# Kernel tuning notes

Measured on AMD Instinct MI355X. Metric: run time of the kernel, lower is better.

Reference implementation:

```python
import jax, jax.numpy as jnp
import numpy as np

EPS = 1e-5

def rmsnorm(x, g):
    var = jnp.mean(jnp.square(x), axis=-1, keepdims=True)
    return x * jax.lax.rsqrt(var + EPS) * g

def setup_inputs() -> dict:
    key = jax.random.key(0)
    ks = jax.random.split(key, 8)
    B, S, T, D = 2, 2048, 2048, 1024
    H, HKV, HD = 16, 4, 64
    std = 0.02
    return {
        "x": jax.random.normal(ks[0], (B, S, D), jnp.float32),
        "kv": jax.random.normal(ks[1], (B, T, D), jnp.float32),
        "wq": jax.random.normal(ks[2], (H * HD, D), jnp.float32) * std,
        "wk": jax.random.normal(ks[3], (HKV * HD, D), jnp.float32) * std,
        "wv": jax.random.normal(ks[4], (HKV * HD, D), jnp.float32) * std,
        "wo": jax.random.normal(ks[5], (D, H * HD), jnp.float32) * std,
        "gq": jnp.ones((D,), jnp.float32),
        "gkv": jnp.ones((D,), jnp.float32),
    }

def reference(x, kv, wq, wk, wv, wo, gq, gkv):
    B, S, D = x.shape
    T = kv.shape[1]
    H, HKV, HD = 16, 4, 64
    R = H // HKV  # heads per kv group
    xn = rmsnorm(x, gq)
    kvn = rmsnorm(kv, gkv)
    # projections
    q = (xn @ wq.T).reshape(B, S, HKV, R, HD)   # grouped query heads
    k = (kvn @ wk.T).reshape(B, T, HKV, HD)
    v = (kvn @ wv.T).reshape(B, T, HKV, HD)
    scale = 1.0 / jnp.sqrt(jnp.float32(HD))
    # block-mask is None -> full dense cross attention; GQA via broadcast einsum
    scores = jnp.einsum('bsgrd,btgd->bgrst', q, k) * scale  # [B,HKV,R,S,T]
    probs = jax.nn.softmax(scores, axis=-1)
    out = jnp.einsum('bgrst,btgd->bsgrd', probs, v)  # [B,S,HKV,R,HD]
    out = out.reshape(B, S, H * HD) @ wo.T
    return x + out
```

## Files before the change

kernel.cpp:

```cpp
#include <hip/hip_runtime.h>

#define DEV __device__ __forceinline__

typedef __attribute__((ext_vector_type(8))) _Float16 h8;
typedef __attribute__((ext_vector_type(4))) float f32x4;

DEV unsigned short f2h(float f) {
  union { _Float16 h[2]; unsigned short u[2]; } v;
  v.h[0] = (_Float16)f;
  return v.u[0];
}

DEV float h2f(unsigned short u) {
  union { _Float16 h[2]; unsigned short u[2]; } v;
  v.u[0] = u;
  return (float)v.h[0];
}

DEV unsigned int pack2h(float a, float b) {
  union { __fp16 __attribute__((ext_vector_type(2))) p; unsigned int u; } v;
  v.p = __builtin_amdgcn_cvt_pkrtz(a, b);
  return v.u;
}

DEV void async_load16(const void* g, void* l) {
  __builtin_amdgcn_global_load_lds(
      (const __attribute__((address_space(1))) void*)g,
      (__attribute__((address_space(3))) void*)l,
      16, 0, 0);
}


__global__ __launch_bounds__(256) void prep(const float* __restrict__ x,
                                            const float* __restrict__ kv,
                                            const float* __restrict__ wq,
                                            const float* __restrict__ wk,
                                            const float* __restrict__ wv,
                                            const float* __restrict__ wo,
                                            const float* __restrict__ gq,
                                            const float* __restrict__ gkv,
                                            unsigned short* __restrict__ wqb,
                                            unsigned short* __restrict__ wkvb,
                                            unsigned short* __restrict__ wob,
                                            unsigned short* __restrict__ xn,
                                            unsigned short* __restrict__ kvn,
                                            float qscale) {
  const int b = blockIdx.x, tid = threadIdx.x;
  if (b < 2560) {
    const float* src;
    unsigned short* dst;
    float sc = 1.0f;
    int base;
    if (b < 1024) { src = wq; dst = wqb; sc = qscale; base = b; }
    else if (b < 1280) { src = wk; dst = wkvb; base = b - 1024; }
    else if (b < 1536) { src = wv; dst = wkvb + 262144; base = b - 1280; }
    else { src = wo; dst = wob; base = b - 1536; }
    const int i = (base * 256 + tid) * 4;
    float4 v = *(const float4*)&src[i];
    ushort4 o;
    o.x = f2h(v.x * sc); o.y = f2h(v.y * sc);
    o.z = f2h(v.z * sc); o.w = f2h(v.w * sc);
    *(ushort4*)&dst[i] = o;
    return;
  }
  int row = b - 2560;
  const float* src;
  const float* g;
  unsigned short* dst;
  if (row < 4096) { src = x; g = gq; dst = xn; }
  else { row -= 4096; src = kv; g = gkv; dst = kvn; }
  const float* xr = src + (size_t)row * 1024;
  float4 v = *(const float4*)&xr[tid * 4];
  float ss = v.x * v.x + v.y * v.y + v.z * v.z + v.w * v.w;
  ss += __shfl_xor(ss, 32); ss += __shfl_xor(ss, 16);
  ss += __shfl_xor(ss, 8);  ss += __shfl_xor(ss, 4);
  ss += __shfl_xor(ss, 2);  ss += __shfl_xor(ss, 1);
  __shared__ float red[4];
  if ((tid & 63) == 0) red[tid >> 6] = ss;
  __syncthreads();
  float tot = red[0] + red[1] + red[2] + red[3];
  float inv = rsqrtf(tot * (1.0f / 1024.0f) + 1e-5f);
  float4 gv = *(const float4*)&g[tid * 4];
  ushort4 o;
  o.x = f2h(v.x * inv * gv.x); o.y = f2h(v.y * inv * gv.y);
  o.z = f2h(v.z * inv * gv.z); o.w = f2h(v.w * inv * gv.w);
  *(ushort4*)&dst[(size_t)row * 1024 + tid * 4] = o;
}

#define GEMM_KLOOP(A_, W_, m0_, n0_, Al_, Bl_, acc_)                                   \
  for (int kk = 0; kk < 1024; kk += 64) {                                              \
    __syncthreads();                                                                   \
    _Pragma("unroll") for (int j = 0; j < 6; ++j) {                                    \
      const int idx = w * 6 + j;                                                       \
      if (idx < 16) {                                                                  \
        const int p = idx >> 3, rb = (idx & 7) * 16;                                   \
        async_load16(A_ + (size_t)(m0_ + rb + r4) * 1024 + kk + p * 32 + c4s,          \
                     &Al_[p][rb * 32]);                                                \
      } else {                                                                         \
        const int ib = idx - 16;                                                       \
        const int p = ib >> 2, rb = (ib & 3) * 16;                                     \
        async_load16(W_ + (size_t)(n0_ + rb + r4) * 1024 + kk + p * 32 + c4s,          \
                     &Bl_[p][rb * 32]);                                                \
      }                                                                                \
    }                                                                                  \
    __syncthreads();                                                                   \
    _Pragma("unroll") for (int kc = 0; kc < 2; ++kc) {                                 \
      h8 af[4], bf[2];                                                                 \
      _Pragma("unroll") for (int mi = 0; mi < 4; ++mi)                                 \
        af[mi] = *(const h8*)&Al_[kc][(wm0 + mi * 16 + ln) * 32 + qs8];                \
      _Pragma("unroll") for (int ni = 0; ni < 2; ++ni)                                 \
        bf[ni] = *(const h8*)&Bl_[kc][(wn0 + ni * 16 + ln) * 32 + qs8];                \
      _Pragma("unroll") for (int mi = 0; mi < 4; ++mi)                                 \
        _Pragma("unroll") for (int ni = 0; ni < 2; ++ni)                               \
          acc_[mi][ni] =                                                               \
              __builtin_amdgcn_mfma_f32_16x16x32_f16(af[mi], bf[ni], acc_[mi][ni],     \
                                                     0, 0, 0);                         \
    }                                                                                  \
  }

__global__ __launch_bounds__(256) void proj_gemm(const unsigned short* __restrict__ xn,
                                                 const unsigned short* __restrict__ kvn,
                                                 const unsigned short* __restrict__ wqb,
                                                 const unsigned short* __restrict__ wkvb,
                                                 unsigned short* __restrict__ qb,
                                                 unsigned short* __restrict__ kb,
                                                 unsigned short* __restrict__ vTb) {
  __shared__ unsigned short Al[2][128 * 32];
  __shared__ unsigned short Bl[2][64 * 32];
  const int tid = threadIdx.x;
  const int w = tid >> 6, l = tid & 63;
  const int quad = l >> 4, ln = l & 15;
  const int wm0 = (w >> 1) * 64, wn0 = (w & 1) * 32;
  const int r4 = l >> 2;
  const int c4s = (((l & 3) ^ ((l >> 3) & 3))) * 8;
  const int qs8 = (quad ^ ((l >> 1) & 3)) * 8;

  int z = blockIdx.x;
  const unsigned short *A, *W;
  int m0, n0, isq;
  if (z < 512) {
    A = xn; W = wqb; isq = 1;
    m0 = (((z >> 7) << 3) + (z & 7)) * 128;
    n0 = ((z >> 3) & 15) * 64;
  } else {
    z -= 512; A = kvn; W = wkvb; isq = 0;
    m0 = (((z >> 6) << 3) + (z & 7)) * 128;
    n0 = ((z >> 3) & 7) * 64;
  }

  f32x4 acc[4][2] = {};
  GEMM_KLOOP(A, W, m0, n0, Al, Bl, acc)

#pragma unroll
  for (int mi = 0; mi < 4; ++mi)
#pragma unroll
    for (int ni = 0; ni < 2; ++ni)
#pragma unroll
      for (int r = 0; r < 4; ++r) {
        const int row = m0 + wm0 + mi * 16 + quad * 4 + r;
        const int col = n0 + wn0 + ni * 16 + ln;
        const unsigned short v = f2h(acc[mi][ni][r]);
        if (isq) {
          qb[((size_t)row << 10) + col] = v;
        } else if (col < 256) {
          kb[(size_t)row * 256 + col] = v;
        } else {
          const int c2 = col - 256, gg = c2 >> 6, dd = c2 & 63;
          const int bb = row >> 11, t = row & 2047;
          vTb[((size_t)((bb * 4 + gg) * 64 + dd) << 11) + t] = v;
        }
      }
}

__global__ __launch_bounds__(256) void o_gemm(const unsigned short* __restrict__ attb,
                                              const unsigned short* __restrict__ wob,
                                              const float* __restrict__ x,
                                              float* __restrict__ out) {
  __shared__ unsigned short Al[2][128 * 32];
  __shared__ unsigned short Bl[2][64 * 32];
  const int tid = threadIdx.x;
  const int w = tid >> 6, l = tid & 63;
  const int quad = l >> 4, ln = l & 15;
  const int wm0 = (w >> 1) * 64, wn0 = (w & 1) * 32;
  const int r4 = l >> 2;
  const int c4s = (((l & 3) ^ ((l >> 3) & 3))) * 8;
  const int qs8 = (quad ^ ((l >> 1) & 3)) * 8;

  const int z = blockIdx.x;
  const int m0 = (((z >> 7) << 3) + (z & 7)) * 128;
  const int n0 = ((z >> 3) & 15) * 64;

  f32x4 acc[4][2] = {};
  GEMM_KLOOP(attb, wob, m0, n0, Al, Bl, acc)

#pragma unroll
  for (int mi = 0; mi < 4; ++mi)
#pragma unroll
    for (int ni = 0; ni < 2; ++ni)
#pragma unroll
      for (int r = 0; r < 4; ++r) {
        const int row = m0 + wm0 + mi * 16 + quad * 4 + r;
        const int col = n0 + wn0 + ni * 16 + ln;
        const size_t idx = ((size_t)row << 10) + col;
        out[idx] = x[idx] + acc[mi][ni][r];
      }
}

__global__ __launch_bounds__(256, 4) void flash_attn(const unsigned short* __restrict__ q,
                                                     const unsigned short* __restrict__ k,
                                                     const unsigned short* __restrict__ vT,
                                                     unsigned short* __restrict__ o0,
                                                     unsigned short* __restrict__ o1,
                                                     float* __restrict__ l0p,
                                                     float* __restrict__ l1p) {
  __shared__ unsigned short KV[4][64 * 32];
  __shared__ unsigned short P[4 * 32 * 72];

  const int tid = threadIdx.x;
  const int w = tid >> 6, l = tid & 63;
  const int quad = l >> 4, ln = l & 15;
  const int s0 = blockIdx.x * 128;
  const int h = blockIdx.y, g = h >> 2;
  const int b = blockIdx.z >> 1, ts = blockIdx.z & 1;
  const int tbase = ts << 10;

  unsigned short* Opart = ts ? o1 : o0;
  float* lpart = ts ? l1p : l0p;

  h8 qf[2][2];
#pragma unroll
  for (int nq = 0; nq < 2; ++nq)
#pragma unroll
    for (int c = 0; c < 2; ++c)
      qf[nq][c] = *(const h8*)&q[(((size_t)(b * 2048 + s0 + w * 32 + nq * 16 + ln)) << 10) +
                                 h * 64 + c * 32 + quad * 8];

  f32x4 oacc[2][4] = {};
  float lsum[2] = {0.0f, 0.0f};

  const unsigned short* kbase = k + ((size_t)(b * 2048)) * 256 + g * 64;
  const unsigned short* vbase = vT + (((size_t)(b * 4 + g) * 64) << 11);
  unsigned short* Pw = &P[w * 32 * 72];

  const int r4 = l >> 2;
  const int c4s = (((l & 3) ^ ((l >> 3) & 3))) * 8;
  const int qs8 = (quad ^ ((l >> 1) & 3)) * 8;

  for (int it = 0; it < 16; ++it) {
    const int t0 = tbase + it * 64;
    __syncthreads();
#pragma unroll
    for (int c = 0; c < 4; ++c) {
      const unsigned short* src;
      if (w < 2)
        src = kbase + (size_t)(t0 + c * 16 + r4) * 256 + w * 32 + c4s;
      else
        src = vbase + (((size_t)(c * 16 + r4)) << 11) + t0 + (w - 2) * 32 + c4s;
      async_load16(src, &KV[w][c * 512]);
    }
    __syncthreads();

    f32x4 st[2][4];
#pragma unroll
    for (int tb = 0; tb < 4; ++tb) {
      h8 ka = *(const h8*)&KV[0][tb * 512 + ln * 32 + qs8];
      h8 kb2 = *(const h8*)&KV[1][tb * 512 + ln * 32 + qs8];
#pragma unroll
      for (int nq = 0; nq < 2; ++nq) {
        f32x4 s = {};
        s = __builtin_amdgcn_mfma_f32_16x16x32_f16(ka, qf[nq][0], s, 0, 0, 0);
        s = __builtin_amdgcn_mfma_f32_16x16x32_f16(kb2, qf[nq][1], s, 0, 0, 0);
        st[nq][tb] = s;
      }
    }

#pragma unroll
    for (int nq = 0; nq < 2; ++nq) {
#pragma unroll
      for (int tb = 0; tb < 4; ++tb) {
        float p0 = __builtin_amdgcn_exp2f(fminf(st[nq][tb][0], 14.0f));
        float p1 = __builtin_amdgcn_exp2f(fminf(st[nq][tb][1], 14.0f));
        float p2 = __builtin_amdgcn_exp2f(fminf(st[nq][tb][2], 14.0f));
        float p3 = __builtin_amdgcn_exp2f(fminf(st[nq][tb][3], 14.0f));
        lsum[nq] += (p0 + p1) + (p2 + p3);
        uint2 pk; pk.x = pack2h(p0, p1); pk.y = pack2h(p2, p3);
        *(uint2*)&Pw[(nq * 16 + ln) * 72 + tb * 16 + quad * 4] = pk;
      }
    }

    asm volatile("s_waitcnt lgkmcnt(0)" ::: "memory");

#pragma unroll
    for (int c = 0; c < 2; ++c) {
      h8 pf0 = *(const h8*)&Pw[(0 * 16 + ln) * 72 + c * 32 + quad * 8];
      h8 pf1 = *(const h8*)&Pw[(1 * 16 + ln) * 72 + c * 32 + quad * 8];
#pragma unroll
      for (int cb = 0; cb < 4; ++cb) {
        h8 vb = *(const h8*)&KV[2 + c][cb * 512 + ln * 32 + qs8];
        oacc[0][cb] = __builtin_amdgcn_mfma_f32_16x16x32_f16(pf0, vb, oacc[0][cb], 0, 0, 0);
        oacc[1][cb] = __builtin_amdgcn_mfma_f32_16x16x32_f16(pf1, vb, oacc[1][cb], 0, 0, 0);
      }
    }
  }

#pragma unroll
  for (int nq = 0; nq < 2; ++nq) {
    lsum[nq] += __shfl_xor(lsum[nq], 16);
    lsum[nq] += __shfl_xor(lsum[nq], 32);
    if (l < 16)
      lpart[(size_t)(b * 2048 + s0 + w * 32 + nq * 16 + l) * 16 + h] = lsum[nq];
#pragma unroll
    for (int r = 0; r < 4; ++r) {
      const size_t row = (size_t)(b * 2048 + s0 + w * 32 + nq * 16 + quad * 4 + r);
#pragma unroll
      for (int cb = 0; cb < 4; ++cb)
        Opart[(row << 10) + h * 64 + cb * 16 + ln] = f2h(oacc[nq][cb][r]);
    }
  }
}

__global__ __launch_bounds__(256) void combine(const unsigned short* __restrict__ O0,
                                               const unsigned short* __restrict__ O1,
                                               const float* __restrict__ l0p,
                                               const float* __restrict__ l1p,
                                               unsigned short* __restrict__ att) {
  const int row = blockIdx.x, tid = threadIdx.x;
  const int col = tid * 4;
  const int h = tid >> 4;
  const float inv = 1.0f / (l0p[row * 16 + h] + l1p[row * 16 + h]);
  const size_t idx = ((size_t)row << 10) + col;
  ushort4 a = *(const ushort4*)&O0[idx];
  ushort4 b = *(const ushort4*)&O1[idx];
  ushort4 o;
  o.x = f2h((h2f(a.x) + h2f(b.x)) * inv);
  o.y = f2h((h2f(a.y) + h2f(b.y)) * inv);
  o.z = f2h((h2f(a.z) + h2f(b.z)) * inv);
  o.w = f2h((h2f(a.w) + h2f(b.w)) * inv);
  *(ushort4*)&att[idx] = o;
}

extern "C" void kernel_launch(void* const* d_in, const int* in_sizes, int n_in,
                              void* d_out, int out_size, void* d_ws, size_t ws_size,
                              hipStream_t stream) {
  const float* x   = (const float*)d_in[0];
  const float* kv  = (const float*)d_in[1];
  const float* wq  = (const float*)d_in[2];
  const float* wk  = (const float*)d_in[3];
  const float* wv  = (const float*)d_in[4];
  const float* wo  = (const float*)d_in[5];
  const float* gq  = (const float*)d_in[6];
  const float* gkv = (const float*)d_in[7];

  char* ws = (char*)d_ws;
  unsigned short* xn   = (unsigned short*)(ws);
  unsigned short* kvn  = (unsigned short*)(ws + 8388608);
  unsigned short* qb   = (unsigned short*)(ws + 16777216);
  unsigned short* kb   = (unsigned short*)(ws + 25165824);
  unsigned short* vTb  = (unsigned short*)(ws + 27262976);
  unsigned short* attb = (unsigned short*)(ws + 29360128);
  unsigned short* wqb  = (unsigned short*)(ws + 37748736);
  unsigned short* wkvb = (unsigned short*)(ws + 39845888);
  unsigned short* wob  = (unsigned short*)(ws + 40894464);
  unsigned short* Opart0 = xn;
  unsigned short* Opart1 = kvn;
  float* l0p = (float*)wqb;
  float* l1p = (float*)(ws + 37748736 + 262144);

  const float qscale = 0.18033688011112042f;

  prep<<<10752, 256, 0, stream>>>(x, kv, wq, wk, wv, wo, gq, gkv,
                                  wqb, wkvb, wob, xn, kvn, qscale);

  proj_gemm<<<768, 256, 0, stream>>>(xn, kvn, wqb, wkvb, qb, kb, vTb);

  flash_attn<<<dim3(16, 16, 4), 256, 0, stream>>>(qb, kb, vTb, Opart0, Opart1, l0p, l1p);
  combine<<<4096, 256, 0, stream>>>(Opart0, Opart1, l0p, l1p, attb);

  o_gemm<<<512, 256, 0, stream>>>(attb, wob, x, (float*)d_out);
}
```

Before: 194.5 us.

## Fuse split-KV combine into O-projection GEMM and double-buffer GEMM K-loops

Removes the separate combine kernel. The O-projection GEMM now loads both partial attention outputs, adds them, scales by the reciprocal softmax sum computed into LDS, and writes the A tile itself. Both GEMMs switch to double-buffered LDS staging, so the next k-tile loads while the current one computes, with one barrier per iteration. The attention kernel drops the exp2 clamp and accumulates row sums with an fp16 dot2 on the packed probabilities. This gains precision-sensitive speed at the cost of summing in fp16, losing overflow protection, and using synchronous A loads in o_gemm.

```diff
diff --git a/kernel.cpp b/kernel.cpp
--- a/kernel.cpp
+++ b/kernel.cpp
@@ -4,6 +4,7 @@
 
 typedef __attribute__((ext_vector_type(8))) _Float16 h8;
 typedef __attribute__((ext_vector_type(4))) float f32x4;
+typedef __fp16 __attribute__((ext_vector_type(2))) hh2;
 
 DEV unsigned short f2h(float f) {
   union { _Float16 h[2]; unsigned short u[2]; } v;
@@ -15,12 +16,6 @@
   union { _Float16 h[2]; unsigned short u[2]; } v;
   v.u[0] = u;
   return (float)v.h[0];
-}
-
-DEV unsigned int pack2h(float a, float b) {
-  union { __fp16 __attribute__((ext_vector_type(2))) p; unsigned int u; } v;
-  v.p = __builtin_amdgcn_cvt_pkrtz(a, b);
-  return v.u;
 }
 
 DEV void async_load16(const void* g, void* l) {
@@ -87,37 +82,6 @@
   *(ushort4*)&dst[(size_t)row * 1024 + tid * 4] = o;
 }
 
-#define GEMM_KLOOP(A_, W_, m0_, n0_, Al_, Bl_, acc_)                                   \
-  for (int kk = 0; kk < 1024; kk += 64) {                                              \
-    __syncthreads();                                                                   \
-    _Pragma("unroll") for (int j = 0; j < 6; ++j) {                                    \
-      const int idx = w * 6 + j;                                                       \
-      if (idx < 16) {                                                                  \
-        const int p = idx >> 3, rb = (idx & 7) * 16;                                   \
-        async_load16(A_ + (size_t)(m0_ + rb + r4) * 1024 + kk + p * 32 + c4s,          \
-                     &Al_[p][rb * 32]);                                                \
-      } else {                                                                         \
-        const int ib = idx - 16;                                                       \
-        const int p = ib >> 2, rb = (ib & 3) * 16;                                     \
-        async_load16(W_ + (size_t)(n0_ + rb + r4) * 1024 + kk + p * 32 + c4s,          \
-                     &Bl_[p][rb * 32]);                                                \
-      }                                                                                \
-    }                                                                                  \
-    __syncthreads();                                                                   \
-    _Pragma("unroll") for (int kc = 0; kc < 2; ++kc) {                                 \
-      h8 af[4], bf[2];                                                                 \
-      _Pragma("unroll") for (int mi = 0; mi < 4; ++mi)                                 \
-        af[mi] = *(const h8*)&Al_[kc][(wm0 + mi * 16 + ln) * 32 + qs8];                \
-      _Pragma("unroll") for (int ni = 0; ni < 2; ++ni)                                 \
-        bf[ni] = *(const h8*)&Bl_[kc][(wn0 + ni * 16 + ln) * 32 + qs8];                \
-      _Pragma("unroll") for (int mi = 0; mi < 4; ++mi)                                 \
-        _Pragma("unroll") for (int ni = 0; ni < 2; ++ni)                               \
-          acc_[mi][ni] =                                                               \
-              __builtin_amdgcn_mfma_f32_16x16x32_f16(af[mi], bf[ni], acc_[mi][ni],     \
-                                                     0, 0, 0);                         \
-    }                                                                                  \
-  }
-
 __global__ __launch_bounds__(256) void proj_gemm(const unsigned short* __restrict__ xn,
                                                  const unsigned short* __restrict__ kvn,
                                                  const unsigned short* __restrict__ wqb,
@@ -125,8 +89,8 @@
                                                  unsigned short* __restrict__ qb,
                                                  unsigned short* __restrict__ kb,
                                                  unsigned short* __restrict__ vTb) {
-  __shared__ unsigned short Al[2][128 * 32];
-  __shared__ unsigned short Bl[2][64 * 32];
+  __shared__ unsigned short Al[2][2][128 * 32];
+  __shared__ unsigned short Bl[2][2][64 * 32];
   const int tid = threadIdx.x;
   const int w = tid >> 6, l = tid & 63;
   const int quad = l >> 4, ln = l & 15;
@@ -149,7 +113,46 @@
   }
 
   f32x4 acc[4][2] = {};
-  GEMM_KLOOP(A, W, m0, n0, Al, Bl, acc)
+
+  auto stage = [&](int buf, int kk) {
+#pragma unroll
+    for (int j = 0; j < 6; ++j) {
+      const int idx = w * 6 + j;
+      if (idx < 16) {
+        const int p = idx >> 3, rb = (idx & 7) * 16;
+        async_load16(A + (size_t)(m0 + rb + r4) * 1024 + kk + p * 32 + c4s,
+                     &Al[buf][p][rb * 32]);
+      } else {
+        const int ib = idx - 16;
+        const int p = ib >> 2, rb = (ib & 3) * 16;
+        async_load16(W + (size_t)(n0 + rb + r4) * 1024 + kk + p * 32 + c4s,
+                     &Bl[buf][p][rb * 32]);
+      }
+    }
+  };
+
+  stage(0, 0);
+#pragma unroll 2
+  for (int it = 0; it < 16; ++it) {
+    const int buf = it & 1;
+    __syncthreads();
+    if (it < 15) stage(buf ^ 1, (it + 1) * 64);
+#pragma unroll
+    for (int kc = 0; kc < 2; ++kc) {
+      h8 af[4], bf[2];
+#pragma unroll
+      for (int mi = 0; mi < 4; ++mi)
+        af[mi] = *(const h8*)&Al[buf][kc][(wm0 + mi * 16 + ln) * 32 + qs8];
+#pragma unroll
+      for (int ni = 0; ni < 2; ++ni)
+        bf[ni] = *(const h8*)&Bl[buf][kc][(wn0 + ni * 16 + ln) * 32 + qs8];
+#pragma unroll
+      for (int mi = 0; mi < 4; ++mi)
+#pragma unroll
+        for (int ni = 0; ni < 2; ++ni)
+          acc[mi][ni] = __builtin_amdgcn_mfma_f32_16x16x32_f16(af[mi], bf[ni], acc[mi][ni], 0, 0, 0);
+    }
+  }
 
 #pragma unroll
   for (int mi = 0; mi < 4; ++mi)
@@ -172,12 +175,16 @@
       }
 }
 
-__global__ __launch_bounds__(256) void o_gemm(const unsigned short* __restrict__ attb,
+__global__ __launch_bounds__(256) void o_gemm(const unsigned short* __restrict__ O0,
+                                              const unsigned short* __restrict__ O1,
+                                              const float* __restrict__ l0p,
+                                              const float* __restrict__ l1p,
                                               const unsigned short* __restrict__ wob,
                                               const float* __restrict__ x,
                                               float* __restrict__ out) {
-  __shared__ unsigned short Al[2][128 * 32];
-  __shared__ unsigned short Bl[2][64 * 32];
+  __shared__ unsigned short Al[2][2][128 * 32];
+  __shared__ unsigned short Bl[2][2][64 * 32];
+  __shared__ float Linv[16 * 128];
   const int tid = threadIdx.x;
   const int w = tid >> 6, l = tid & 63;
   const int quad = l >> 4, ln = l & 15;
@@ -190,8 +197,70 @@
   const int m0 = (((z >> 7) << 3) + (z & 7)) * 128;
   const int n0 = ((z >> 3) & 15) * 64;
 
+  {
+    const int h = tid >> 4, r0 = (tid & 15) * 8;
+#pragma unroll
+    for (int i = 0; i < 8; ++i) {
+      const int r = r0 + i;
+      const size_t li = (size_t)(m0 + r) * 16 + h;
+      Linv[h * 128 + r] = 1.0f / (l0p[li] + l1p[li]);
+    }
+  }
+  __syncthreads();
+
+  const int srow = tid >> 3;
+  const int sp = (tid >> 2) & 1;
+  const int ss = tid & 3;
+
+  auto stageA = [&](int buf, int kk) {
+    const int h = kk >> 6;
+#pragma unroll
+    for (int ps = 0; ps < 4; ++ps) {
+      const int row = ps * 32 + srow;
+      const size_t gidx = (size_t)(m0 + row) * 1024 + kk + sp * 32 + ss * 8;
+      h8 a0 = *(const h8*)&O0[gidx];
+      h8 a1 = *(const h8*)&O1[gidx];
+      const _Float16 lv = (_Float16)Linv[h * 128 + row];
+      h8 sum = a0 + a1;
+#pragma unroll
+      for (int q2 = 0; q2 < 8; ++q2) sum[q2] *= lv;
+      const int sl = ss ^ ((row >> 1) & 3);
+      *(h8*)&Al[buf][sp][row * 32 + sl * 8] = sum;
+    }
+  };
+  auto stageB = [&](int buf, int kk) {
+#pragma unroll
+    for (int j = 0; j < 2; ++j) {
+      const int ib = w * 2 + j;
+      const int p = ib >> 2, rb = (ib & 3) * 16;
+      async_load16(wob + (size_t)(n0 + rb + r4) * 1024 + kk + p * 32 + c4s,
+                   &Bl[buf][p][rb * 32]);
+    }
+  };
+
   f32x4 acc[4][2] = {};
-  GEMM_KLOOP(attb, wob, m0, n0, Al, Bl, acc)
+  stageB(0, 0);
+  stageA(0, 0);
+  for (int it = 0; it < 16; ++it) {
+    const int buf = it & 1;
+    __syncthreads();
+    if (it < 15) { stageB(buf ^ 1, (it + 1) * 64); stageA(buf ^ 1, (it + 1) * 64); }
+#pragma unroll
+    for (int kc = 0; kc < 2; ++kc) {
+      h8 af[4], bf[2];
+#pragma unroll
+      for (int mi = 0; mi < 4; ++mi)
+        af[mi] = *(const h8*)&Al[buf][kc][(wm0 + mi * 16 + ln) * 32 + qs8];
+#pragma unroll
+      for (int ni = 0; ni < 2; ++ni)
+        bf[ni] = *(const h8*)&Bl[buf][kc][(wn0 + ni * 16 + ln) * 32 + qs8];
+#pragma unroll
+      for (int mi = 0; mi < 4; ++mi)
+#pragma unroll
+        for (int ni = 0; ni < 2; ++ni)
+          acc[mi][ni] = __builtin_amdgcn_mfma_f32_16x16x32_f16(af[mi], bf[ni], acc[mi][ni], 0, 0, 0);
+    }
+  }
 
 #pragma unroll
   for (int mi = 0; mi < 4; ++mi)
@@ -246,6 +315,8 @@
   const int c4s = (((l & 3) ^ ((l >> 3) & 3))) * 8;
   const int qs8 = (quad ^ ((l >> 1) & 3)) * 8;
 
+  const hh2 one2 = {(__fp16)1.0f, (__fp16)1.0f};
+
   for (int it = 0; it < 16; ++it) {
     const int t0 = tbase + it * 64;
     __syncthreads();
@@ -278,12 +349,20 @@
     for (int nq = 0; nq < 2; ++nq) {
 #pragma unroll
       for (int tb = 0; tb < 4; ++tb) {
-        float p0 = __builtin_amdgcn_exp2f(fminf(st[nq][tb][0], 14.0f));
-        float p1 = __builtin_amdgcn_exp2f(fminf(st[nq][tb][1], 14.0f));
-        float p2 = __builtin_amdgcn_exp2f(fminf(st[nq][tb][2], 14.0f));
-        float p3 = __builtin_amdgcn_exp2f(fminf(st[nq][tb][3], 14.0f));
+        float p0 = __builtin_amdgcn_exp2f(st[nq][tb][0]);
+        float p1 = __builtin_amdgcn_exp2f(st[nq][tb][1]);
+        float p2 = __builtin_amdgcn_exp2f(st[nq][tb][2]);
+        float p3 = __builtin_amdgcn_exp2f(st[nq][tb][3]);
+        union { hh2 h2; unsigned int u; } pa, pb;
+        pa.h2 = __builtin_amdgcn_cvt_pkrtz(p0, p1);
+        pb.h2 = __builtin_amdgcn_cvt_pkrtz(p2, p3);
+#if __has_builtin(__builtin_amdgcn_fdot2)
+        lsum[nq] = __builtin_amdgcn_fdot2(pa.h2, one2, lsum[nq], false);
+        lsum[nq] = __builtin_amdgcn_fdot2(pb.h2, one2, lsum[nq], false);
+#else
         lsum[nq] += (p0 + p1) + (p2 + p3);
-        uint2 pk; pk.x = pack2h(p0, p1); pk.y = pack2h(p2, p3);
+#endif
+        uint2 pk; pk.x = pa.u; pk.y = pb.u;
         *(uint2*)&Pw[(nq * 16 + ln) * 72 + tb * 16 + quad * 4] = pk;
       }
     }
@@ -317,26 +396,6 @@
         Opart[(row << 10) + h * 64 + cb * 16 + ln] = f2h(oacc[nq][cb][r]);
     }
   }
-}
-
-__global__ __launch_bounds__(256) void combine(const unsigned short* __restrict__ O0,
-                                               const unsigned short* __restrict__ O1,
-                                               const float* __restrict__ l0p,
-                                               const float* __restrict__ l1p,
-                                               unsigned short* __restrict__ att) {
-  const int row = blockIdx.x, tid = threadIdx.x;
-  const int col = tid * 4;
-  const int h = tid >> 4;
-  const float inv = 1.0f / (l0p[row * 16 + h] + l1p[row * 16 + h]);
-  const size_t idx = ((size_t)row << 10) + col;
-  ushort4 a = *(const ushort4*)&O0[idx];
-  ushort4 b = *(const ushort4*)&O1[idx];
-  ushort4 o;
-  o.x = f2h((h2f(a.x) + h2f(b.x)) * inv);
-  o.y = f2h((h2f(a.y) + h2f(b.y)) * inv);
-  o.z = f2h((h2f(a.z) + h2f(b.z)) * inv);
-  o.w = f2h((h2f(a.w) + h2f(b.w)) * inv);
-  *(ushort4*)&att[idx] = o;
 }
 
 extern "C" void kernel_launch(void* const* d_in, const int* in_sizes, int n_in,
@@ -357,7 +416,6 @@
   unsigned short* qb   = (unsigned short*)(ws + 16777216);
   unsigned short* kb   = (unsigned short*)(ws + 25165824);
   unsigned short* vTb  = (unsigned short*)(ws + 27262976);
-  unsigned short* attb = (unsigned short*)(ws + 29360128);
   unsigned short* wqb  = (unsigned short*)(ws + 37748736);
   unsigned short* wkvb = (unsigned short*)(ws + 39845888);
   unsigned short* wob  = (unsigned short*)(ws + 40894464);
@@ -374,7 +432,6 @@
   proj_gemm<<<768, 256, 0, stream>>>(xn, kvn, wqb, wkvb, qb, kb, vTb);
 
   flash_attn<<<dim3(16, 16, 4), 256, 0, stream>>>(qb, kb, vTb, Opart0, Opart1, l0p, l1p);
-  combine<<<4096, 256, 0, stream>>>(Opart0, Opart1, l0p, l1p, attb);
-
-  o_gemm<<<512, 256, 0, stream>>>(attb, wob, x, (float*)d_out);
-}
+
+  o_gemm<<<512, 256, 0, stream>>>(Opart0, Opart1, l0p, l1p, wob, x, (float*)d_out);
+}
```

Measured after the change: 190.9 us. About the same (-1.9%).
